# Performance work log

Measured on AMD Instinct MI355X. Metric: run time of the kernel, lower is better.

The kernel has to match this reference:

```python
import jax, jax.numpy as jnp
import numpy as np

IN_FEATURES = 128
DEPTH = 2
UNITS = 512
BATCH = 2048
W_SCALE = 0.02


def _create_masks():
    degrees = [np.arange(IN_FEATURES)]
    for _ in range(DEPTH):
        degrees.append(np.arange(UNITS) % (IN_FEATURES - 1))
    degrees.append(degrees[0] % IN_FEATURES - 1)
    masks = []
    for d1, d2 in zip(degrees[:-1], degrees[1:]):
        masks.append(np.greater_equal(d2[:, None], d1[None, :]).astype('float32'))
    masks[-1] = np.tile(masks[-1], (2, 1))  # final layer outputs [mu; sigma]
    return masks


def setup_inputs() -> dict:
    key = jax.random.key(0)
    ks = jax.random.split(key, 7)
    m1, m2, m3 = _create_masks()
    u = jax.random.normal(ks[0], (BATCH, IN_FEATURES), dtype=jnp.float32)
    # torch.nn.Linear weight layout: [out_features, in_features]
    W1 = jax.random.normal(ks[1], (UNITS, IN_FEATURES), dtype=jnp.float32) * W_SCALE
    b1 = jax.random.normal(ks[2], (UNITS,), dtype=jnp.float32) * W_SCALE
    W2 = jax.random.normal(ks[3], (UNITS, UNITS), dtype=jnp.float32) * W_SCALE
    b2 = jax.random.normal(ks[4], (UNITS,), dtype=jnp.float32) * W_SCALE
    W3 = jax.random.normal(ks[5], (2 * IN_FEATURES, UNITS), dtype=jnp.float32) * W_SCALE
    b3 = jax.random.normal(ks[6], (2 * IN_FEATURES,), dtype=jnp.float32) * W_SCALE
    return {
        'u': u,
        'W1': W1, 'b1': b1, 'W2': W2, 'b2': b2, 'W3': W3, 'b3': b3,
        'mask1': jnp.asarray(m1), 'mask2': jnp.asarray(m2), 'mask3': jnp.asarray(m3),
    }


def reference(u, W1, b1, W2, b2, W3, b3, mask1, mask2, mask3):
    # Pre-apply masks once; math identical to masking inside every step.
    mW1 = mask1 * W1
    mW2 = mask2 * W2
    mW3 = mask3 * W3

    def conditioner(x):
        h = jax.nn.relu(x @ mW1.T + b1)
        h = jax.nn.relu(h @ mW2.T + b2)
        z = h @ mW3.T + b3  # [B, 2*IN_FEATURES]
        return z[:, :IN_FEATURES], z[:, IN_FEATURES:]  # mu, sigma

    def step(x, i):
        mu, sigma = conditioner(x)
        mu_i = jnp.take(mu, i, axis=1)        # [B]
        sig_i = jnp.take(sigma, i, axis=1)    # [B]
        u_i = jnp.take(u, i, axis=1)          # [B]
        x = x.at[:, i].set(u_i * jnp.exp(sig_i) + mu_i)
        return x, sig_i

    x0 = jnp.zeros_like(u)
    x, sigs = jax.lax.scan(step, x0, jnp.arange(IN_FEATURES))
    # sigs: [IN_FEATURES, B]; log_det_jacobian = sum_i sigma_i -> [B, 1]
    log_det_jacobian = jnp.sum(sigs, axis=0)[:, None]
    return x, log_det_jacobian
```

## Files before the change

kernel.cpp:

```cpp
#include <hip/hip_runtime.h>
#include <hip/hip_fp16.h>
#include <math.h>

static constexpr int BATCH = 2048;

static constexpr int STEP_BYTES = 7168;
static constexpr int X2_FOFF    = 227584;
static constexpr int X3_FOFF    = X2_FOFF + 2048;

__device__ __forceinline__ int sigmaInvU(int s) {
    int i = s >> 2, t = s & 3;
    return (i == 127) ? (508 + t) : (127 * t + i);
}
__device__ __forceinline__ int degU(int x) {
    return (x < 508) ? (x % 127) : (x - 508);
}
__device__ __forceinline__ float fc(float4 v, int k) {
    return k == 0 ? v.x : k == 1 ? v.y : k == 2 ? v.z : v.w;
}
__device__ __forceinline__ unsigned uc(uint4 v, int k) {
    return k == 0 ? v.x : k == 1 ? v.y : k == 2 ? v.z : v.w;
}
__device__ __forceinline__ float hlo(unsigned u) {
    return __half2float(__ushort_as_half((unsigned short)(u & 0xffffu)));
}
__device__ __forceinline__ float hhi(unsigned u) {
    return __half2float(__ushort_as_half((unsigned short)(u >> 16)));
}
__device__ __forceinline__ float rl(float v, int l) {
    return __int_as_float(__builtin_amdgcn_readlane(__float_as_int(v), l));
}

__global__ __launch_bounds__(256) void maf_prep(
    const float* __restrict__ W1, const float* __restrict__ W2,
    const float* __restrict__ W3, float* __restrict__ ws)
{
    const int NCH = 127 * 448;
    int q = blockIdx.x * 256 + threadIdx.x;
    if (q < NCH) {
        int i = q / 448, rem = q % 448;
        unsigned short h[8];
        if (rem < 128) {
            int L = rem >> 1, f = rem & 1;
#pragma unroll
            for (int e = 0; e < 8; ++e) {
                int t = 2 * f + (e >> 2), c = e & 3;
                int cu = 127 * c + L;
                float v = (L >= i) ? W2[cu * 512 + 127 * t + i] : 0.f;
                h[e] = __half_as_ushort(__float2half(v));
            }
        } else if (rem < 192) {
            int L = rem - 128;
#pragma unroll
            for (int e = 0; e < 8; ++e) {
                int s = (e < 4) ? (4 * L + e) : (256 + 4 * L + (e - 4));
                int cu = sigmaInvU(s);
                int dg = degU(cu);
                float v = (dg >= i) ? W1[cu * 128 + i] : 0.f;
                h[e] = __half_as_ushort(__float2half(v));
            }
        } else if (rem < 320) {
            int idx = rem - 192, L = idx >> 1, f = idx & 1;
#pragma unroll
            for (int e = 0; e < 8; ++e) {
                int t = 2 * f + (e >> 2), c = e & 3;
                int cu = sigmaInvU(256 + 4 * L + c);
                int dg = degU(cu);
                float v = (dg >= i) ? W2[cu * 512 + 127 * t + i] : 0.f;
                h[e] = __half_as_ushort(__float2half(v));
            }
        } else {
            int idx = rem - 320, L = idx >> 1, f = idx & 1;
#pragma unroll
            for (int e = 0; e < 8; ++e) {
                int t = 2 * f + (e >> 2), c = e & 3;
                int o = 4 * L + c;
                float v = ((o & 127) - 1 >= i) ? W3[o * 512 + 127 * t + i] : 0.f;
                h[e] = __half_as_ushort(__float2half(v));
            }
        }
        uint4 o4;
        o4.x = (unsigned)h[0] | ((unsigned)h[1] << 16);
        o4.y = (unsigned)h[2] | ((unsigned)h[3] << 16);
        o4.z = (unsigned)h[4] | ((unsigned)h[5] << 16);
        o4.w = (unsigned)h[6] | ((unsigned)h[7] << 16);
        *(uint4*)((char*)ws + (size_t)q * 16) = o4;
    } else if (q < NCH + 768) {
        int e = q - NCH;
        if (e < 512) {
            int t = e >> 7, s0 = (e & 127) * 4;
            float4 o4;
#pragma unroll
            for (int c = 0; c < 4; ++c) {
                int cu = sigmaInvU(s0 + c);
                float v = (degU(cu) >= t) ? W2[cu * 512 + 508 + t] : 0.f;
                if (c == 0) o4.x = v; else if (c == 1) o4.y = v;
                else if (c == 2) o4.z = v; else o4.w = v;
            }
            *(float4*)(ws + X2_FOFF + t * 512 + s0) = o4;
        } else {
            int e2 = e - 512;
            int t = e2 >> 6, o0 = (e2 & 63) * 4;
            float4 o4;
#pragma unroll
            for (int c = 0; c < 4; ++c) {
                int o = o0 + c;
                float v = ((o & 127) - 1 >= t) ? W3[o * 512 + 508 + t] : 0.f;
                if (c == 0) o4.x = v; else if (c == 1) o4.y = v;
                else if (c == 2) o4.z = v; else o4.w = v;
            }
            *(float4*)(ws + X3_FOFF + t * 256 + o0) = o4;
        }
    }
}

#define DECL_WSET(P) \
    uint4 P##a0{}, P##a1{}, P##b0{}, P##b1{}, P##b2{}, P##b3{}, P##b4{};

#define LOADS_LO(P) do { \
    P##a0 = *(const uint4*)(pA); \
    P##a1 = *(const uint4*)(pA + 16); \
    P##b0 = *(const uint4*)(pB0); \
    P##b1 = *(const uint4*)(pB12); \
    P##b2 = *(const uint4*)(pB12 + 16); \
    P##b3 = *(const uint4*)(pB34); \
    P##b4 = *(const uint4*)(pB34 + 16); \
    pA += STEP_BYTES; pB0 += STEP_BYTES; pB12 += STEP_BYTES; pB34 += STEP_BYTES; \
    __builtin_amdgcn_sched_barrier(0); \
} while (0)

#define LOADS_HI(P) do { \
    P##b0 = *(const uint4*)(pB0); \
    P##b1 = *(const uint4*)(pB12); \
    P##b2 = *(const uint4*)(pB12 + 16); \
    P##b3 = *(const uint4*)(pB34); \
    P##b4 = *(const uint4*)(pB34 + 16); \
    pA += STEP_BYTES; pB0 += STEP_BYTES; pB12 += STEP_BYTES; pB34 += STEP_BYTES; \
    __builtin_amdgcn_sched_barrier(0); \
} while (0)

#define L2ONE(P, T, LO) do { \
    const float hA = rl(fmaxf(LO ? h1A[T] : h1A[4 + (T)], 0.f), l0); \
    const float hB = rl(fmaxf(LO ? h1B[T] : h1B[4 + (T)], 0.f), l0); \
    if (LO) { \
        const unsigned m0 = uc((T) < 2 ? P##a0 : P##a1, 2 * ((T) & 1)); \
        const unsigned m1 = uc((T) < 2 ? P##a0 : P##a1, 2 * ((T) & 1) + 1); \
        h2A[0] = fmaf(hlo(m0), hA, h2A[0]); h2A[1] = fmaf(hhi(m0), hA, h2A[1]); \
        h2A[2] = fmaf(hlo(m1), hA, h2A[2]); h2A[3] = fmaf(hhi(m1), hA, h2A[3]); \
        h2B[0] = fmaf(hlo(m0), hB, h2B[0]); h2B[1] = fmaf(hhi(m0), hB, h2B[1]); \
        h2B[2] = fmaf(hlo(m1), hB, h2B[2]); h2B[3] = fmaf(hhi(m1), hB, h2B[3]); \
    } \
    const unsigned n0 = uc((T) < 2 ? P##b1 : P##b2, 2 * ((T) & 1)); \
    const unsigned n1 = uc((T) < 2 ? P##b1 : P##b2, 2 * ((T) & 1) + 1); \
    h2A[4] = fmaf(hlo(n0), hA, h2A[4]); h2A[5] = fmaf(hhi(n0), hA, h2A[5]); \
    h2A[6] = fmaf(hlo(n1), hA, h2A[6]); h2A[7] = fmaf(hhi(n1), hA, h2A[7]); \
    h2B[4] = fmaf(hlo(n0), hB, h2B[4]); h2B[5] = fmaf(hhi(n0), hB, h2B[5]); \
    h2B[6] = fmaf(hlo(n1), hB, h2B[6]); h2B[7] = fmaf(hhi(n1), hB, h2B[7]); \
} while (0)

#define L3ONE(P, T, LO) do { \
    const float gA = rl(fmaxf(LO ? h2A[T] : h2A[4 + (T)], 0.f), l0); \
    const float gB = rl(fmaxf(LO ? h2B[T] : h2B[4 + (T)], 0.f), l0); \
    const unsigned p0 = uc((T) < 2 ? P##b3 : P##b4, 2 * ((T) & 1)); \
    const unsigned p1 = uc((T) < 2 ? P##b3 : P##b4, 2 * ((T) & 1) + 1); \
    zA[0] = fmaf(hlo(p0), gA, zA[0]); zA[1] = fmaf(hhi(p0), gA, zA[1]); \
    zA[2] = fmaf(hlo(p1), gA, zA[2]); zA[3] = fmaf(hhi(p1), gA, zA[3]); \
    zB[0] = fmaf(hlo(p0), gB, zB[0]); zB[1] = fmaf(hhi(p0), gB, zB[1]); \
    zB[2] = fmaf(hlo(p1), gB, zB[2]); zB[3] = fmaf(hhi(p1), gB, zB[3]); \
} while (0)

#define STEP(I, P, LO) do { \
    const int l0 = (I) & 63, lm = (I) >> 2, rs = (I) & 3; \
    float zsA = rs == 0 ? zA[0] : rs == 1 ? zA[1] : rs == 2 ? zA[2] : zA[3]; \
    float zsB = rs == 0 ? zB[0] : rs == 1 ? zB[1] : rs == 2 ? zB[2] : zB[3]; \
    const float muA = rl(zsA, lm), sgA = rl(zsA, 32 + lm); \
    const float muB = rl(zsB, lm), sgB = rl(zsB, 32 + lm); \
    const float uiA = rl(LO ? uA0 : uA1, l0); \
    const float uiB = rl(LO ? uB0 : uB1, l0); \
    const float xiA = fmaf(uiA, __expf(sgA), muA); \
    const float xiB = fmaf(uiB, __expf(sgB), muB); \
    ldA += sgA; ldB += sgB; \
    if (lane == l0) { \
        if (LO) { xA0 = xiA; xB0 = xiB; } else { xA1 = xiA; xB1 = xiB; } \
    } \
    if (LO) { \
        h1A[0] = fmaf(hlo(P##b0.x), xiA, h1A[0]); \
        h1A[1] = fmaf(hhi(P##b0.x), xiA, h1A[1]); \
        h1A[2] = fmaf(hlo(P##b0.y), xiA, h1A[2]); \
        h1A[3] = fmaf(hhi(P##b0.y), xiA, h1A[3]); \
        h1B[0] = fmaf(hlo(P##b0.x), xiB, h1B[0]); \
        h1B[1] = fmaf(hhi(P##b0.x), xiB, h1B[1]); \
        h1B[2] = fmaf(hlo(P##b0.y), xiB, h1B[2]); \
        h1B[3] = fmaf(hhi(P##b0.y), xiB, h1B[3]); \
    } \
    h1A[4] = fmaf(hlo(P##b0.z), xiA, h1A[4]); \
    h1A[5] = fmaf(hhi(P##b0.z), xiA, h1A[5]); \
    h1A[6] = fmaf(hlo(P##b0.w), xiA, h1A[6]); \
    h1A[7] = fmaf(hhi(P##b0.w), xiA, h1A[7]); \
    h1B[4] = fmaf(hlo(P##b0.z), xiB, h1B[4]); \
    h1B[5] = fmaf(hhi(P##b0.z), xiB, h1B[5]); \
    h1B[6] = fmaf(hlo(P##b0.w), xiB, h1B[6]); \
    h1B[7] = fmaf(hhi(P##b0.w), xiB, h1B[7]); \
    L2ONE(P, 0, LO); L2ONE(P, 1, LO); L2ONE(P, 2, LO); L2ONE(P, 3, LO); \
    if (LO && (I) < 4) { \
        float eA = (I) == 0 ? h1A[4] : (I) == 1 ? h1A[5] : (I) == 2 ? h1A[6] : h1A[7]; \
        float eB = (I) == 0 ? h1B[4] : (I) == 1 ? h1B[5] : (I) == 2 ? h1B[6] : h1B[7]; \
        const float hA = rl(fmaxf(eA, 0.f), 63); \
        const float hB = rl(fmaxf(eB, 0.f), 63); \
        const float4 wl = *(const float4*)(P2X + (I) * 512 + 4 * lane); \
        const float4 wh = *(const float4*)(P2X + (I) * 512 + 256 + 4 * lane); \
        _Pragma("unroll") for (int r = 0; r < 4; ++r) { \
            h2A[r] = fmaf(fc(wl, r), hA, h2A[r]); \
            h2B[r] = fmaf(fc(wl, r), hB, h2B[r]); \
            h2A[4 + r] = fmaf(fc(wh, r), hA, h2A[4 + r]); \
            h2B[4 + r] = fmaf(fc(wh, r), hB, h2B[4 + r]); } \
    } \
    L3ONE(P, 0, LO); L3ONE(P, 1, LO); L3ONE(P, 2, LO); L3ONE(P, 3, LO); \
    if (LO && (I) < 4) { \
        float eA = (I) == 0 ? h2A[4] : (I) == 1 ? h2A[5] : (I) == 2 ? h2A[6] : h2A[7]; \
        float eB = (I) == 0 ? h2B[4] : (I) == 1 ? h2B[5] : (I) == 2 ? h2B[6] : h2B[7]; \
        const float gA = rl(fmaxf(eA, 0.f), 63); \
        const float gB = rl(fmaxf(eB, 0.f), 63); \
        const float4 w4 = *(const float4*)(P3X + (I) * 256 + 4 * lane); \
        _Pragma("unroll") for (int s = 0; s < 4; ++s) { \
            zA[s] = fmaf(fc(w4, s), gA, zA[s]); \
            zB[s] = fmaf(fc(w4, s), gB, zB[s]); } \
    } \
} while (0)

__global__ __launch_bounds__(256, 1) void maf_inverse(
    const float* __restrict__ u, const float* __restrict__ b1,
    const float* __restrict__ b2, const float* __restrict__ b3,
    const float* __restrict__ ws, float* __restrict__ out)
{
    const float* P2X = ws + X2_FOFF;
    const float* P3X = ws + X3_FOFF;

    const int td = threadIdx.x;
    const int lane = td & 63;
    const int wid = td >> 6;
    const int rA = blockIdx.x * 8 + wid * 2;
    const int rB = rA + 1;

    float h1A[8], h1B[8], h2A[8], h2B[8];
#pragma unroll
    for (int r = 0; r < 8; ++r) {
        int s = (r < 4) ? (4 * lane + r) : (256 + 4 * lane + (r - 4));
        int uu = sigmaInvU(s);
        float v1 = b1[uu], v2 = b2[uu];
        h1A[r] = v1; h1B[r] = v1; h2A[r] = v2; h2B[r] = v2;
    }
    float zA[4], zB[4];
    {
        const float4 bz = *(const float4*)(b3 + 4 * lane);
        zA[0] = bz.x; zA[1] = bz.y; zA[2] = bz.z; zA[3] = bz.w;
        zB[0] = bz.x; zB[1] = bz.y; zB[2] = bz.z; zB[3] = bz.w;
    }
    const float uA0 = u[rA * 128 + lane], uA1 = u[rA * 128 + 64 + lane];
    const float uB0 = u[rB * 128 + lane], uB1 = u[rB * 128 + 64 + lane];

    float xA0 = 0.f, xA1 = 0.f, xB0 = 0.f, xB1 = 0.f, ldA = 0.f, ldB = 0.f;

    const char* pA   = (const char*)ws + 32 * lane;
    const char* pB0  = (const char*)ws + 2048 + 16 * lane;
    const char* pB12 = (const char*)ws + 3072 + 32 * lane;
    const char* pB34 = (const char*)ws + 5120 + 32 * lane;

    DECL_WSET(wa)
    DECL_WSET(wb)

    LOADS_LO(wa);
#pragma unroll 1
    for (int i = 0; i < 62; i += 2) {
        LOADS_LO(wb);
        STEP(i, wa, true);
        LOADS_LO(wa);
        STEP(i + 1, wb, true);
    }
    LOADS_LO(wb);
    STEP(62, wa, true);
    LOADS_HI(wa);
    STEP(63, wb, true);
#pragma unroll 1
    for (int i = 64; i < 126; i += 2) {
        LOADS_HI(wb);
        STEP(i, wa, false);
        LOADS_HI(wa);
        STEP(i + 1, wb, false);
    }
    STEP(126, wa, false);

    {
        const float muA = rl(zA[3], 31), sgA = rl(zA[3], 63);
        const float muB = rl(zB[3], 31), sgB = rl(zB[3], 63);
        const float uiA = rl(uA1, 63), uiB = rl(uB1, 63);
        const float xiA = fmaf(uiA, __expf(sgA), muA);
        const float xiB = fmaf(uiB, __expf(sgB), muB);
        ldA += sgA; ldB += sgB;
        if (lane == 63) { xA1 = xiA; xB1 = xiB; }
    }

    out[rA * 128 + lane]      = xA0;
    out[rA * 128 + 64 + lane] = xA1;
    out[rB * 128 + lane]      = xB0;
    out[rB * 128 + 64 + lane] = xB1;
    if (lane == 0) {
        out[BATCH * 128 + rA] = ldA;
        out[BATCH * 128 + rB] = ldB;
    }
}

extern "C" void kernel_launch(void* const* d_in, const int* in_sizes, int n_in,
                              void* d_out, int out_size, void* d_ws, size_t ws_size,
                              hipStream_t stream)
{
    const float* u  = (const float*)d_in[0];
    const float* W1 = (const float*)d_in[1];
    const float* b1 = (const float*)d_in[2];
    const float* W2 = (const float*)d_in[3];
    const float* b2 = (const float*)d_in[4];
    const float* W3 = (const float*)d_in[5];
    const float* b3 = (const float*)d_in[6];
    float* ws  = (float*)d_ws;
    float* out = (float*)d_out;
    (void)ws_size; (void)in_sizes; (void)n_in; (void)out_size;

    maf_prep<<<226, 256, 0, stream>>>(W1, W2, W3, ws);
    maf_inverse<<<256, 256, 0, stream>>>(u, b1, b2, b3, ws, out);
}
```

Measured before the change: 137.2 us.

## Assign one batch row per wavefront and double the grid to 512 blocks

Each wavefront now handles a single batch row instead of two, and the grid doubles to 512 blocks with launch bounds raised to allow two blocks per CU. The per-step weight loads are now shared by half as many rows, so total weight traffic from cache doubles. In exchange, per-thread registers are roughly halved and there are twice as many wavefronts to hide the latency of the serial 128-step dependency chain. The four walking weight pointers are also replaced by one base pointer with fixed lane offsets, which saves a few address registers and adds.

```diff
diff --git a/kernel.cpp b/kernel.cpp
--- a/kernel.cpp
+++ b/kernel.cpp
@@ -118,117 +118,88 @@
     uint4 P##a0{}, P##a1{}, P##b0{}, P##b1{}, P##b2{}, P##b3{}, P##b4{};
 
 #define LOADS_LO(P) do { \
-    P##a0 = *(const uint4*)(pA); \
-    P##a1 = *(const uint4*)(pA + 16); \
-    P##b0 = *(const uint4*)(pB0); \
-    P##b1 = *(const uint4*)(pB12); \
-    P##b2 = *(const uint4*)(pB12 + 16); \
-    P##b3 = *(const uint4*)(pB34); \
-    P##b4 = *(const uint4*)(pB34 + 16); \
-    pA += STEP_BYTES; pB0 += STEP_BYTES; pB12 += STEP_BYTES; pB34 += STEP_BYTES; \
+    P##a0 = *(const uint4*)(sb + offA); \
+    P##a1 = *(const uint4*)(sb + offA + 16); \
+    P##b0 = *(const uint4*)(sb + offB1); \
+    P##b1 = *(const uint4*)(sb + offB2); \
+    P##b2 = *(const uint4*)(sb + offB2 + 16); \
+    P##b3 = *(const uint4*)(sb + offB3); \
+    P##b4 = *(const uint4*)(sb + offB3 + 16); \
+    sb += STEP_BYTES; \
     __builtin_amdgcn_sched_barrier(0); \
 } while (0)
 
 #define LOADS_HI(P) do { \
-    P##b0 = *(const uint4*)(pB0); \
-    P##b1 = *(const uint4*)(pB12); \
-    P##b2 = *(const uint4*)(pB12 + 16); \
-    P##b3 = *(const uint4*)(pB34); \
-    P##b4 = *(const uint4*)(pB34 + 16); \
-    pA += STEP_BYTES; pB0 += STEP_BYTES; pB12 += STEP_BYTES; pB34 += STEP_BYTES; \
+    P##b0 = *(const uint4*)(sb + offB1); \
+    P##b1 = *(const uint4*)(sb + offB2); \
+    P##b2 = *(const uint4*)(sb + offB2 + 16); \
+    P##b3 = *(const uint4*)(sb + offB3); \
+    P##b4 = *(const uint4*)(sb + offB3 + 16); \
+    sb += STEP_BYTES; \
     __builtin_amdgcn_sched_barrier(0); \
 } while (0)
 
 #define L2ONE(P, T, LO) do { \
-    const float hA = rl(fmaxf(LO ? h1A[T] : h1A[4 + (T)], 0.f), l0); \
-    const float hB = rl(fmaxf(LO ? h1B[T] : h1B[4 + (T)], 0.f), l0); \
+    const float hv = rl(fmaxf(LO ? h1[T] : h1[4 + (T)], 0.f), l0); \
     if (LO) { \
         const unsigned m0 = uc((T) < 2 ? P##a0 : P##a1, 2 * ((T) & 1)); \
         const unsigned m1 = uc((T) < 2 ? P##a0 : P##a1, 2 * ((T) & 1) + 1); \
-        h2A[0] = fmaf(hlo(m0), hA, h2A[0]); h2A[1] = fmaf(hhi(m0), hA, h2A[1]); \
-        h2A[2] = fmaf(hlo(m1), hA, h2A[2]); h2A[3] = fmaf(hhi(m1), hA, h2A[3]); \
-        h2B[0] = fmaf(hlo(m0), hB, h2B[0]); h2B[1] = fmaf(hhi(m0), hB, h2B[1]); \
-        h2B[2] = fmaf(hlo(m1), hB, h2B[2]); h2B[3] = fmaf(hhi(m1), hB, h2B[3]); \
+        h2[0] = fmaf(hlo(m0), hv, h2[0]); h2[1] = fmaf(hhi(m0), hv, h2[1]); \
+        h2[2] = fmaf(hlo(m1), hv, h2[2]); h2[3] = fmaf(hhi(m1), hv, h2[3]); \
     } \
     const unsigned n0 = uc((T) < 2 ? P##b1 : P##b2, 2 * ((T) & 1)); \
     const unsigned n1 = uc((T) < 2 ? P##b1 : P##b2, 2 * ((T) & 1) + 1); \
-    h2A[4] = fmaf(hlo(n0), hA, h2A[4]); h2A[5] = fmaf(hhi(n0), hA, h2A[5]); \
-    h2A[6] = fmaf(hlo(n1), hA, h2A[6]); h2A[7] = fmaf(hhi(n1), hA, h2A[7]); \
-    h2B[4] = fmaf(hlo(n0), hB, h2B[4]); h2B[5] = fmaf(hhi(n0), hB, h2B[5]); \
-    h2B[6] = fmaf(hlo(n1), hB, h2B[6]); h2B[7] = fmaf(hhi(n1), hB, h2B[7]); \
+    h2[4] = fmaf(hlo(n0), hv, h2[4]); h2[5] = fmaf(hhi(n0), hv, h2[5]); \
+    h2[6] = fmaf(hlo(n1), hv, h2[6]); h2[7] = fmaf(hhi(n1), hv, h2[7]); \
 } while (0)
 
 #define L3ONE(P, T, LO) do { \
-    const float gA = rl(fmaxf(LO ? h2A[T] : h2A[4 + (T)], 0.f), l0); \
-    const float gB = rl(fmaxf(LO ? h2B[T] : h2B[4 + (T)], 0.f), l0); \
+    const float gv = rl(fmaxf(LO ? h2[T] : h2[4 + (T)], 0.f), l0); \
     const unsigned p0 = uc((T) < 2 ? P##b3 : P##b4, 2 * ((T) & 1)); \
     const unsigned p1 = uc((T) < 2 ? P##b3 : P##b4, 2 * ((T) & 1) + 1); \
-    zA[0] = fmaf(hlo(p0), gA, zA[0]); zA[1] = fmaf(hhi(p0), gA, zA[1]); \
-    zA[2] = fmaf(hlo(p1), gA, zA[2]); zA[3] = fmaf(hhi(p1), gA, zA[3]); \
-    zB[0] = fmaf(hlo(p0), gB, zB[0]); zB[1] = fmaf(hhi(p0), gB, zB[1]); \
-    zB[2] = fmaf(hlo(p1), gB, zB[2]); zB[3] = fmaf(hhi(p1), gB, zB[3]); \
+    z[0] = fmaf(hlo(p0), gv, z[0]); z[1] = fmaf(hhi(p0), gv, z[1]); \
+    z[2] = fmaf(hlo(p1), gv, z[2]); z[3] = fmaf(hhi(p1), gv, z[3]); \
 } while (0)
 
 #define STEP(I, P, LO) do { \
     const int l0 = (I) & 63, lm = (I) >> 2, rs = (I) & 3; \
-    float zsA = rs == 0 ? zA[0] : rs == 1 ? zA[1] : rs == 2 ? zA[2] : zA[3]; \
-    float zsB = rs == 0 ? zB[0] : rs == 1 ? zB[1] : rs == 2 ? zB[2] : zB[3]; \
-    const float muA = rl(zsA, lm), sgA = rl(zsA, 32 + lm); \
-    const float muB = rl(zsB, lm), sgB = rl(zsB, 32 + lm); \
-    const float uiA = rl(LO ? uA0 : uA1, l0); \
-    const float uiB = rl(LO ? uB0 : uB1, l0); \
-    const float xiA = fmaf(uiA, __expf(sgA), muA); \
-    const float xiB = fmaf(uiB, __expf(sgB), muB); \
-    ldA += sgA; ldB += sgB; \
-    if (lane == l0) { \
-        if (LO) { xA0 = xiA; xB0 = xiB; } else { xA1 = xiA; xB1 = xiB; } \
-    } \
+    float zs = rs == 0 ? z[0] : rs == 1 ? z[1] : rs == 2 ? z[2] : z[3]; \
+    const float mu = rl(zs, lm), sg = rl(zs, 32 + lm); \
+    const float ui = rl(LO ? u0 : u1, l0); \
+    const float xi = fmaf(ui, __expf(sg), mu); \
+    ld += sg; \
+    if (lane == l0) { if (LO) x0 = xi; else x1 = xi; } \
     if (LO) { \
-        h1A[0] = fmaf(hlo(P##b0.x), xiA, h1A[0]); \
-        h1A[1] = fmaf(hhi(P##b0.x), xiA, h1A[1]); \
-        h1A[2] = fmaf(hlo(P##b0.y), xiA, h1A[2]); \
-        h1A[3] = fmaf(hhi(P##b0.y), xiA, h1A[3]); \
-        h1B[0] = fmaf(hlo(P##b0.x), xiB, h1B[0]); \
-        h1B[1] = fmaf(hhi(P##b0.x), xiB, h1B[1]); \
-        h1B[2] = fmaf(hlo(P##b0.y), xiB, h1B[2]); \
-        h1B[3] = fmaf(hhi(P##b0.y), xiB, h1B[3]); \
-    } \
-    h1A[4] = fmaf(hlo(P##b0.z), xiA, h1A[4]); \
-    h1A[5] = fmaf(hhi(P##b0.z), xiA, h1A[5]); \
-    h1A[6] = fmaf(hlo(P##b0.w), xiA, h1A[6]); \
-    h1A[7] = fmaf(hhi(P##b0.w), xiA, h1A[7]); \
-    h1B[4] = fmaf(hlo(P##b0.z), xiB, h1B[4]); \
-    h1B[5] = fmaf(hhi(P##b0.z), xiB, h1B[5]); \
-    h1B[6] = fmaf(hlo(P##b0.w), xiB, h1B[6]); \
-    h1B[7] = fmaf(hhi(P##b0.w), xiB, h1B[7]); \
+        h1[0] = fmaf(hlo(P##b0.x), xi, h1[0]); \
+        h1[1] = fmaf(hhi(P##b0.x), xi, h1[1]); \
+        h1[2] = fmaf(hlo(P##b0.y), xi, h1[2]); \
+        h1[3] = fmaf(hhi(P##b0.y), xi, h1[3]); \
+    } \
+    h1[4] = fmaf(hlo(P##b0.z), xi, h1[4]); \
+    h1[5] = fmaf(hhi(P##b0.z), xi, h1[5]); \
+    h1[6] = fmaf(hlo(P##b0.w), xi, h1[6]); \
+    h1[7] = fmaf(hhi(P##b0.w), xi, h1[7]); \
     L2ONE(P, 0, LO); L2ONE(P, 1, LO); L2ONE(P, 2, LO); L2ONE(P, 3, LO); \
     if (LO && (I) < 4) { \
-        float eA = (I) == 0 ? h1A[4] : (I) == 1 ? h1A[5] : (I) == 2 ? h1A[6] : h1A[7]; \
-        float eB = (I) == 0 ? h1B[4] : (I) == 1 ? h1B[5] : (I) == 2 ? h1B[6] : h1B[7]; \
-        const float hA = rl(fmaxf(eA, 0.f), 63); \
-        const float hB = rl(fmaxf(eB, 0.f), 63); \
+        float e1 = (I) == 0 ? h1[4] : (I) == 1 ? h1[5] : (I) == 2 ? h1[6] : h1[7]; \
+        const float hv = rl(fmaxf(e1, 0.f), 63); \
         const float4 wl = *(const float4*)(P2X + (I) * 512 + 4 * lane); \
         const float4 wh = *(const float4*)(P2X + (I) * 512 + 256 + 4 * lane); \
         _Pragma("unroll") for (int r = 0; r < 4; ++r) { \
-            h2A[r] = fmaf(fc(wl, r), hA, h2A[r]); \
-            h2B[r] = fmaf(fc(wl, r), hB, h2B[r]); \
-            h2A[4 + r] = fmaf(fc(wh, r), hA, h2A[4 + r]); \
-            h2B[4 + r] = fmaf(fc(wh, r), hB, h2B[4 + r]); } \
+            h2[r] = fmaf(fc(wl, r), hv, h2[r]); \
+            h2[4 + r] = fmaf(fc(wh, r), hv, h2[4 + r]); } \
     } \
     L3ONE(P, 0, LO); L3ONE(P, 1, LO); L3ONE(P, 2, LO); L3ONE(P, 3, LO); \
     if (LO && (I) < 4) { \
-        float eA = (I) == 0 ? h2A[4] : (I) == 1 ? h2A[5] : (I) == 2 ? h2A[6] : h2A[7]; \
-        float eB = (I) == 0 ? h2B[4] : (I) == 1 ? h2B[5] : (I) == 2 ? h2B[6] : h2B[7]; \
-        const float gA = rl(fmaxf(eA, 0.f), 63); \
-        const float gB = rl(fmaxf(eB, 0.f), 63); \
+        float e2 = (I) == 0 ? h2[4] : (I) == 1 ? h2[5] : (I) == 2 ? h2[6] : h2[7]; \
+        const float gv = rl(fmaxf(e2, 0.f), 63); \
         const float4 w4 = *(const float4*)(P3X + (I) * 256 + 4 * lane); \
-        _Pragma("unroll") for (int s = 0; s < 4; ++s) { \
-            zA[s] = fmaf(fc(w4, s), gA, zA[s]); \
-            zB[s] = fmaf(fc(w4, s), gB, zB[s]); } \
-    } \
-} while (0)
-
-__global__ __launch_bounds__(256, 1) void maf_inverse(
+        _Pragma("unroll") for (int s = 0; s < 4; ++s) \
+            z[s] = fmaf(fc(w4, s), gv, z[s]); \
+    } \
+} while (0)
+
+__global__ __launch_bounds__(256, 2) void maf_inverse(
     const float* __restrict__ u, const float* __restrict__ b1,
     const float* __restrict__ b2, const float* __restrict__ b3,
     const float* __restrict__ ws, float* __restrict__ out)
@@ -239,32 +210,28 @@
     const int td = threadIdx.x;
     const int lane = td & 63;
     const int wid = td >> 6;
-    const int rA = blockIdx.x * 8 + wid * 2;
-    const int rB = rA + 1;
-
-    float h1A[8], h1B[8], h2A[8], h2B[8];
+    const int row = blockIdx.x * 4 + wid;
+
+    float h1[8], h2[8], z[4];
 #pragma unroll
     for (int r = 0; r < 8; ++r) {
         int s = (r < 4) ? (4 * lane + r) : (256 + 4 * lane + (r - 4));
         int uu = sigmaInvU(s);
-        float v1 = b1[uu], v2 = b2[uu];
-        h1A[r] = v1; h1B[r] = v1; h2A[r] = v2; h2B[r] = v2;
-    }
-    float zA[4], zB[4];
+        h1[r] = b1[uu]; h2[r] = b2[uu];
+    }
     {
         const float4 bz = *(const float4*)(b3 + 4 * lane);
-        zA[0] = bz.x; zA[1] = bz.y; zA[2] = bz.z; zA[3] = bz.w;
-        zB[0] = bz.x; zB[1] = bz.y; zB[2] = bz.z; zB[3] = bz.w;
-    }
-    const float uA0 = u[rA * 128 + lane], uA1 = u[rA * 128 + 64 + lane];
-    const float uB0 = u[rB * 128 + lane], uB1 = u[rB * 128 + 64 + lane];
-
-    float xA0 = 0.f, xA1 = 0.f, xB0 = 0.f, xB1 = 0.f, ldA = 0.f, ldB = 0.f;
-
-    const char* pA   = (const char*)ws + 32 * lane;
-    const char* pB0  = (const char*)ws + 2048 + 16 * lane;
-    const char* pB12 = (const char*)ws + 3072 + 32 * lane;
-    const char* pB34 = (const char*)ws + 5120 + 32 * lane;
+        z[0] = bz.x; z[1] = bz.y; z[2] = bz.z; z[3] = bz.w;
+    }
+    const float u0 = u[row * 128 + lane], u1 = u[row * 128 + 64 + lane];
+
+    float x0 = 0.f, x1 = 0.f, ld = 0.f;
+
+    const char* sb = (const char*)ws;
+    const int offA  = 32 * lane;
+    const int offB1 = 2048 + 16 * lane;
+    const int offB2 = 3072 + 32 * lane;
+    const int offB3 = 5120 + 32 * lane;
 
     DECL_WSET(wa)
     DECL_WSET(wb)
@@ -291,23 +258,16 @@
     STEP(126, wa, false);
 
     {
-        const float muA = rl(zA[3], 31), sgA = rl(zA[3], 63);
-        const float muB = rl(zB[3], 31), sgB = rl(zB[3], 63);
-        const float uiA = rl(uA1, 63), uiB = rl(uB1, 63);
-        const float xiA = fmaf(uiA, __expf(sgA), muA);
-        const float xiB = fmaf(uiB, __expf(sgB), muB);
-        ldA += sgA; ldB += sgB;
-        if (lane == 63) { xA1 = xiA; xB1 = xiB; }
-    }
-
-    out[rA * 128 + lane]      = xA0;
-    out[rA * 128 + 64 + lane] = xA1;
-    out[rB * 128 + lane]      = xB0;
-    out[rB * 128 + 64 + lane] = xB1;
-    if (lane == 0) {
-        out[BATCH * 128 + rA] = ldA;
-        out[BATCH * 128 + rB] = ldB;
-    }
+        const float mu = rl(z[3], 31), sg = rl(z[3], 63);
+        const float ui = rl(u1, 63);
+        const float xi = fmaf(ui, __expf(sg), mu);
+        ld += sg;
+        if (lane == 63) x1 = xi;
+    }
+
+    out[row * 128 + lane]      = x0;
+    out[row * 128 + 64 + lane] = x1;
+    if (lane == 0) out[BATCH * 128 + row] = ld;
 }
 
 extern "C" void kernel_launch(void* const* d_in, const int* in_sizes, int n_in,
@@ -326,5 +286,5 @@
     (void)ws_size; (void)in_sizes; (void)n_in; (void)out_size;
 
     maf_prep<<<226, 256, 0, stream>>>(W1, W2, W3, ws);
-    maf_inverse<<<256, 256, 0, stream>>>(u, b1, b2, b3, ws, out);
-}
+    maf_inverse<<<512, 256, 0, stream>>>(u, b1, b2, b3, ws, out);
+}
```

Result: slower. 144.6 us (+5.4%).
